# Optimization experiments

Measured on AMD Instinct MI355X. Metric: run time of the kernel, lower is better.

Reference implementation:

```python
import jax, jax.numpy as jnp
import numpy as np

N_NODES = 100000
NFEAT, NHID, NCLASS, HEADS = 256, 16, 40, 8
NEG_SLOPE = 0.2


def gat_conv(x, src, dst, W, att_src, att_dst, bias, n_nodes):
    """PyG-style GATConv (concat heads). x:[N,Fin], src/dst:[E] (self-loops included)."""
    H, C = att_src.shape
    h = (x @ W).reshape(n_nodes, H, C)                      # [N,H,C]
    a_src = jnp.einsum('nhc,hc->nh', h, att_src)            # [N,H]
    a_dst = jnp.einsum('nhc,hc->nh', h, att_dst)            # [N,H]
    e = jax.nn.leaky_relu(a_src[src] + a_dst[dst], NEG_SLOPE)  # [E,H]
    # segment softmax over edges grouped by destination node
    emax = jax.ops.segment_max(e, dst, num_segments=n_nodes)
    emax = jnp.where(jnp.isfinite(emax), emax, 0.0)
    ex = jnp.exp(e - emax[dst])
    denom = jax.ops.segment_sum(ex, dst, num_segments=n_nodes)
    alpha = ex / (denom[dst] + 1e-16)                       # [E,H]
    msg = h[src] * alpha[:, :, None]                        # [E,H,C] gather + weight
    out = jax.ops.segment_sum(msg, dst, num_segments=n_nodes)  # [N,H,C]
    return out.reshape(n_nodes, H * C) + bias


def setup_inputs() -> dict:
    key = jax.random.key(0)
    ks = jax.random.split(key, 12)
    E = 1600000
    x = jax.random.normal(ks[0], (N_NODES, NFEAT), dtype=jnp.float32)
    edge_index = jax.random.randint(ks[1], (2, E), 0, N_NODES, dtype=jnp.int64)
    s = 0.05
    W1 = jax.random.normal(ks[2], (NFEAT, HEADS * NHID), dtype=jnp.float32) * s
    att_src1 = jax.random.normal(ks[3], (HEADS, NHID), dtype=jnp.float32) * s
    att_dst1 = jax.random.normal(ks[4], (HEADS, NHID), dtype=jnp.float32) * s
    b1 = jnp.zeros((HEADS * NHID,), dtype=jnp.float32)
    W2 = jax.random.normal(ks[5], (HEADS * NHID, NCLASS), dtype=jnp.float32) * s
    att_src2 = jax.random.normal(ks[6], (1, NCLASS), dtype=jnp.float32) * s
    att_dst2 = jax.random.normal(ks[7], (1, NCLASS), dtype=jnp.float32) * s
    b2 = jnp.zeros((NCLASS,), dtype=jnp.float32)
    return {"x": x, "edge_index": edge_index, "W1": W1, "att_src1": att_src1,
            "att_dst1": att_dst1, "b1": b1, "W2": W2, "att_src2": att_src2,
            "att_dst2": att_dst2, "b2": b2}


def reference(x, edge_index, W1, att_src1, att_dst1, b1, W2, att_src2, att_dst2, b2):
    n = x.shape[0]
    # PyG GATConv adds self-loops by default
    loop = jnp.arange(n, dtype=edge_index.dtype)
    src = jnp.concatenate([edge_index[0], loop])
    dst = jnp.concatenate([edge_index[1], loop])
    h = gat_conv(x, src, dst, W1, att_src1, att_dst1, b1, n)
    h = jax.nn.relu(h)  # activation='relu'; dropout/bn are identity in eval / use_bn=False
    out = gat_conv(h, src, dst, W2, att_src2, att_dst2, b2, n)
    return out
```

## Files before the change

### kernel.cpp

```cpp
#include <hip/hip_runtime.h>
#include <math.h>

#define KF 256
#define F1 128
#define NH 8
#define NC 16
#define NCLS 40
#define NEG 0.2f
#define BM 64

static __device__ __forceinline__ float lrelu(float v) { return fmaxf(v, NEG * v); }

static __device__ __forceinline__ unsigned bf16r(float a) {
    unsigned u = __float_as_uint(a);
    return (u + 0x7fffu + ((u >> 16) & 1u)) >> 16;
}
static __device__ __forceinline__ unsigned bf16pack2(float a, float b) {
    return bf16r(a) | (bf16r(b) << 16);
}
static __device__ __forceinline__ float2 bf2unpack(unsigned v) {
    float2 r;
    r.x = __uint_as_float(v << 16);
    r.y = __uint_as_float(v & 0xffff0000u);
    return r;
}

typedef __attribute__((ext_vector_type(8))) short bf16x8;
typedef __attribute__((ext_vector_type(4))) float f32x4;

__global__ __launch_bounds__(256) void wprep_kernel(const float* __restrict__ W1,
                                                    unsigned short* __restrict__ wfrag)
{
    int gid = blockIdx.x * 256 + threadIdx.x;
    if (gid >= KF * F1) return;
    int k = gid >> 7, nn = gid & 127;
    int kt = k >> 6, ks = (k >> 5) & 1, oct = (k >> 3) & 3, e = k & 7;
    int nt = nn >> 4, ln = (nn & 15) + 16 * oct;
    int idx = (((kt * 8 + nt) * 2 + ks) * 64 + ln) * 8 + e;
    wfrag[idx] = (unsigned short)bf16r(W1[gid]);
}

__global__ __launch_bounds__(256) void gemm1_kernel(const float* __restrict__ x,
        const unsigned short* __restrict__ wfrag,
        const float* __restrict__ att_src, const float* __restrict__ att_dst,
        unsigned short* __restrict__ h1u, float* __restrict__ a_src, float* __restrict__ a_dst, int n)
{
    __shared__ __align__(16) unsigned short Al[4096];
    __shared__ __align__(16) unsigned short Bl[8192];
    const int t = threadIdx.x;
    const int w = t >> 6, lane = t & 63;
    const int row0 = blockIdx.x * BM;

    f32x4 acc[8];
#pragma unroll
    for (int i = 0; i < 8; ++i) acc[i] = (f32x4){0.f, 0.f, 0.f, 0.f};

    for (int kt = 0; kt < 4; ++kt) {
        {
            const int k4 = t & 15;
            const int ks = k4 >> 3;
            const int oct = (k4 >> 1) & 3;
            const int koff = (k4 & 1) * 4;
#pragma unroll
            for (int it = 0; it < 4; ++it) {
                int r = (t >> 4) + it * 16;
                int gr = row0 + r;
                float4 v = make_float4(0.f, 0.f, 0.f, 0.f);
                if (gr < n) v = *(const float4*)&x[(size_t)gr * KF + kt * 64 + k4 * 4];
                int ln = (r & 15) + 16 * oct;
                int rt = r >> 4;
                int idx = ((rt * 2 + ks) * 64 + ln) * 8 + koff;
                uint2 p;
                p.x = bf16pack2(v.x, v.y);
                p.y = bf16pack2(v.z, v.w);
                *(uint2*)&Al[idx] = p;
            }
        }
        {
            const uint4* src = (const uint4*)wfrag + kt * 1024;
            uint4* dstp = (uint4*)Bl;
#pragma unroll
            for (int i = 0; i < 4; ++i) dstp[t + i * 256] = src[t + i * 256];
        }
        __syncthreads();
        bf16x8 a0 = *(const bf16x8*)&Al[(w * 2 + 0) * 512 + lane * 8];
        bf16x8 a1 = *(const bf16x8*)&Al[(w * 2 + 1) * 512 + lane * 8];
#pragma unroll
        for (int nt = 0; nt < 8; ++nt) {
            bf16x8 b0 = *(const bf16x8*)&Bl[(nt * 2 + 0) * 512 + lane * 8];
            bf16x8 b1 = *(const bf16x8*)&Bl[(nt * 2 + 1) * 512 + lane * 8];
            acc[nt] = __builtin_amdgcn_mfma_f32_16x16x32_bf16(a0, b0, acc[nt], 0, 0, 0);
            acc[nt] = __builtin_amdgcn_mfma_f32_16x16x32_bf16(a1, b1, acc[nt], 0, 0, 0);
        }
        __syncthreads();
    }

    const int col = lane & 15, g = lane >> 4;
    const int rbase = row0 + w * 16 + g * 4;
#pragma unroll
    for (int nt = 0; nt < 8; ++nt) {
        float asv = att_src[nt * 16 + col];
        float adv = att_dst[nt * 16 + col];
#pragma unroll
        for (int reg = 0; reg < 4; ++reg) {
            int row = rbase + reg;
            float hv = acc[nt][reg];
            if (row < n) h1u[(size_t)row * F1 + nt * 16 + col] = (unsigned short)bf16r(hv);
            float ps = hv * asv, pd = hv * adv;
            ps += __shfl_xor(ps, 1); ps += __shfl_xor(ps, 2);
            ps += __shfl_xor(ps, 4); ps += __shfl_xor(ps, 8);
            pd += __shfl_xor(pd, 1); pd += __shfl_xor(pd, 2);
            pd += __shfl_xor(pd, 4); pd += __shfl_xor(pd, 8);
            if (col == 0 && row < n) {
                a_src[row * NH + nt] = ps;
                a_dst[row * NH + nt] = pd;
            }
        }
    }
}

__global__ __launch_bounds__(256) void histrank_kernel(const int* __restrict__ ei, int E, int Etot,
                                                       int* __restrict__ counts,
                                                       int* __restrict__ rank)
{
    const int base = blockIdx.x * 2048 + threadIdx.x;
#pragma unroll
    for (int q = 0; q < 8; ++q) {
        int i = base + q * 256;
        if (i < Etot) {
            int dst = (i < E) ? ei[E + i] : (i - E);
            rank[i] = atomicAdd(&counts[dst], 1);
        }
    }
}

__global__ __launch_bounds__(256) void scan1_kernel(const int* __restrict__ counts,
                                                    int* __restrict__ bsum, int n)
{
    __shared__ int lds[256];
    const int t = threadIdx.x;
    const int base = blockIdx.x * 1024 + t * 4;
    int s = 0;
#pragma unroll
    for (int q = 0; q < 4; ++q) { int i = base + q; if (i < n) s += counts[i]; }
    lds[t] = s;
    __syncthreads();
#pragma unroll
    for (int off = 128; off > 0; off >>= 1) {
        if (t < off) lds[t] += lds[t + off];
        __syncthreads();
    }
    if (t == 0) bsum[blockIdx.x] = lds[0];
}

__global__ __launch_bounds__(256) void scan2_kernel(const int* __restrict__ bsum,
                                                    int* __restrict__ boffs, int nb,
                                                    int* __restrict__ indptr, int n, int Etot)
{
    __shared__ int lds[256];
    const int t = threadIdx.x;
    lds[t] = (t < nb) ? bsum[t] : 0;
    __syncthreads();
    for (int off = 1; off < 256; off <<= 1) {
        int v = (t >= off) ? lds[t - off] : 0;
        __syncthreads();
        lds[t] += v;
        __syncthreads();
    }
    if (t < nb) boffs[t] = (t == 0) ? 0 : lds[t - 1];
    if (t == 0) indptr[n] = Etot;
}

__global__ __launch_bounds__(256) void scan3_kernel(const int* __restrict__ counts,
                                                    const int* __restrict__ boffs,
                                                    int* __restrict__ indptr, int n)
{
    __shared__ int lds[256];
    const int t = threadIdx.x;
    const int base = blockIdx.x * 1024 + t * 4;
    int c[4];
    int s = 0;
#pragma unroll
    for (int q = 0; q < 4; ++q) {
        int i = base + q;
        c[q] = (i < n) ? counts[i] : 0;
        s += c[q];
    }
    lds[t] = s;
    __syncthreads();
    for (int off = 1; off < 256; off <<= 1) {
        int v = (t >= off) ? lds[t - off] : 0;
        __syncthreads();
        lds[t] += v;
        __syncthreads();
    }
    int run = boffs[blockIdx.x] + lds[t] - s;
#pragma unroll
    for (int q = 0; q < 4; ++q) {
        int i = base + q;
        if (i < n) indptr[i] = run;
        run += c[q];
    }
}

__global__ __launch_bounds__(256) void fill_kernel(const int* __restrict__ ei, int E, int Etot,
                                                   const int* __restrict__ indptr,
                                                   const int* __restrict__ rank,
                                                   int* __restrict__ sorted_src)
{
    const int base = blockIdx.x * 2048 + threadIdx.x;
#pragma unroll
    for (int q = 0; q < 8; ++q) {
        int i = base + q * 256;
        if (i < Etot) {
            int src, dst;
            if (i < E) { src = ei[i]; dst = ei[E + i]; }
            else       { src = i - E; dst = i - E; }
            sorted_src[indptr[dst] + rank[i]] = src;
        }
    }
}

__global__ __launch_bounds__(256) void agg1_kernel(const unsigned* __restrict__ h1b,
        const float* __restrict__ a_src, const float* __restrict__ a_dst,
        const int* __restrict__ indptr, const int* __restrict__ ssrc,
        const float* __restrict__ b1, unsigned* __restrict__ out1b, int n)
{
    const int wave = threadIdx.x >> 6, lane = threadIdx.x & 63;
    const int dst = blockIdx.x * 4 + wave;
    if (dst >= n) return;
    const int h = lane >> 3;
    const float ad = a_dst[dst * NH + h];
    const int beg = indptr[dst], end = indptr[dst + 1];
    float s0 = 0.f, s1 = 0.f, s2 = 0.f, s3 = 0.f;
    float ax0 = 0.f, ay0 = 0.f, ax1 = 0.f, ay1 = 0.f;
    float ax2 = 0.f, ay2 = 0.f, ax3 = 0.f, ay3 = 0.f;
    int j = beg;
    for (; j + 4 <= end; j += 4) {
        int sc0 = ssrc[j], sc1 = ssrc[j + 1], sc2 = ssrc[j + 2], sc3 = ssrc[j + 3];
        float as0 = a_src[sc0 * NH + h];
        float as1 = a_src[sc1 * NH + h];
        float as2 = a_src[sc2 * NH + h];
        float as3 = a_src[sc3 * NH + h];
        unsigned v0 = h1b[(size_t)sc0 * 64 + lane];
        unsigned v1 = h1b[(size_t)sc1 * 64 + lane];
        unsigned v2 = h1b[(size_t)sc2 * 64 + lane];
        unsigned v3 = h1b[(size_t)sc3 * 64 + lane];
        float p0 = __expf(lrelu(as0 + ad));
        float p1 = __expf(lrelu(as1 + ad));
        float p2 = __expf(lrelu(as2 + ad));
        float p3 = __expf(lrelu(as3 + ad));
        float2 hv0 = bf2unpack(v0), hv1 = bf2unpack(v1);
        float2 hv2 = bf2unpack(v2), hv3 = bf2unpack(v3);
        s0 += p0; ax0 += p0 * hv0.x; ay0 += p0 * hv0.y;
        s1 += p1; ax1 += p1 * hv1.x; ay1 += p1 * hv1.y;
        s2 += p2; ax2 += p2 * hv2.x; ay2 += p2 * hv2.y;
        s3 += p3; ax3 += p3 * hv3.x; ay3 += p3 * hv3.y;
    }
    for (; j < end; ++j) {
        int sc = ssrc[j];
        float as = a_src[sc * NH + h];
        float2 hv = bf2unpack(h1b[(size_t)sc * 64 + lane]);
        float p = __expf(lrelu(as + ad));
        s0 += p; ax0 += p * hv.x; ay0 += p * hv.y;
    }
    float s = (s0 + s1) + (s2 + s3);
    float accx = (ax0 + ax1) + (ax2 + ax3);
    float accy = (ay0 + ay1) + (ay2 + ay3);
    float inv = 1.f / (s + 1e-16f);
    float2 bb = *(const float2*)&b1[lane * 2];
    float ox = fmaxf(accx * inv + bb.x, 0.f);
    float oy = fmaxf(accy * inv + bb.y, 0.f);
    out1b[(size_t)dst * 64 + lane] = bf16pack2(ox, oy);
}

__global__ __launch_bounds__(256) void gemm2_kernel(const unsigned* __restrict__ out1b,
        const float* __restrict__ W2, const float* __restrict__ atts2,
        const float* __restrict__ attd2,
        unsigned short* __restrict__ h2us, float* __restrict__ a_src, float* __restrict__ a_dst, int n)
{
    __shared__ float wl[128][NCLS];
    __shared__ float xs[64][68];
    const int t = threadIdx.x;
    const int row0 = blockIdx.x * 64;
    const int rg = t >> 3;
    const int cg = t & 7;
    const int r0 = rg * 2;

#pragma unroll
    for (int i = t; i < 1280; i += 256)
        *(float4*)&wl[0][0 + i * 4] = *(const float4*)&W2[i * 4];

    float acc[2][5];
#pragma unroll
    for (int i = 0; i < 2; ++i)
#pragma unroll
        for (int j = 0; j < 5; ++j) acc[i][j] = 0.f;

    for (int kh = 0; kh < 2; ++kh) {
#pragma unroll
        for (int i = t; i < 1024; i += 256) {
            int r = i >> 4, u2 = i & 15;
            int gr = row0 + r;
            float4 v = make_float4(0.f, 0.f, 0.f, 0.f);
            if (gr < n) {
                uint2 pk = *(const uint2*)&out1b[(size_t)gr * 64 + kh * 32 + u2 * 2];
                float2 ab = bf2unpack(pk.x);
                float2 cd = bf2unpack(pk.y);
                v = make_float4(ab.x, ab.y, cd.x, cd.y);
            }
            *(float4*)&xs[r][u2 * 4] = v;
        }
        __syncthreads();
#pragma unroll 4
        for (int k = 0; k < 64; ++k) {
            float xa = xs[r0][k];
            float xb = xs[r0 + 1][k];
            const float* wr = &wl[kh * 64 + k][cg * 5];
#pragma unroll
            for (int j = 0; j < 5; ++j) {
                float w = wr[j];
                acc[0][j] += xa * w;
                acc[1][j] += xb * w;
            }
        }
        __syncthreads();
    }

    float as5[5], ad5[5];
#pragma unroll
    for (int j = 0; j < 5; ++j) {
        as5[j] = atts2[cg * 5 + j];
        ad5[j] = attd2[cg * 5 + j];
    }
#pragma unroll
    for (int i = 0; i < 2; ++i) {
        int row = row0 + r0 + i;
        if (row >= n) break;
#pragma unroll
        for (int j = 0; j < 5; ++j)
            h2us[(size_t)row * NCLS + cg * 5 + j] = (unsigned short)bf16r(acc[i][j]);
        float ps = acc[i][0] * as5[0] + acc[i][1] * as5[1] + acc[i][2] * as5[2]
                 + acc[i][3] * as5[3] + acc[i][4] * as5[4];
        float pd = acc[i][0] * ad5[0] + acc[i][1] * ad5[1] + acc[i][2] * ad5[2]
                 + acc[i][3] * ad5[3] + acc[i][4] * ad5[4];
        ps += __shfl_xor(ps, 1); ps += __shfl_xor(ps, 2); ps += __shfl_xor(ps, 4);
        pd += __shfl_xor(pd, 1); pd += __shfl_xor(pd, 2); pd += __shfl_xor(pd, 4);
        if (cg == 0) { a_src[row] = ps; a_dst[row] = pd; }
    }
}

__global__ __launch_bounds__(256) void agg2_kernel(const unsigned* __restrict__ h2b,
        const float* __restrict__ a_src, const float* __restrict__ a_dst,
        const int* __restrict__ indptr, const int* __restrict__ ssrc,
        const float* __restrict__ b2, float* __restrict__ out, int n)
{
    const int wave = threadIdx.x >> 6, lane = threadIdx.x & 63;
    const int grp = lane / 20;
    const int sub = lane - grp * 20;
    const int dst = blockIdx.x * 12 + wave * 3 + grp;
    const bool valid = (grp < 3) && (dst < n);
    const float ad = valid ? a_dst[dst] : 0.f;
    int beg = 0, end = 0;
    if (valid) { beg = indptr[dst]; end = indptr[dst + 1]; }
    float s0 = 0.f, s1 = 0.f, s2 = 0.f, s3 = 0.f;
    float ax0 = 0.f, ay0 = 0.f, ax1 = 0.f, ay1 = 0.f;
    float ax2 = 0.f, ay2 = 0.f, ax3 = 0.f, ay3 = 0.f;
    int j = beg;
    for (; j + 4 <= end; j += 4) {
        int sc0 = ssrc[j], sc1 = ssrc[j + 1], sc2 = ssrc[j + 2], sc3 = ssrc[j + 3];
        float p0 = __expf(lrelu(a_src[sc0] + ad));
        float p1 = __expf(lrelu(a_src[sc1] + ad));
        float p2 = __expf(lrelu(a_src[sc2] + ad));
        float p3 = __expf(lrelu(a_src[sc3] + ad));
        float2 h0 = bf2unpack(h2b[(size_t)sc0 * 20 + sub]);
        float2 h1v = bf2unpack(h2b[(size_t)sc1 * 20 + sub]);
        float2 h2v = bf2unpack(h2b[(size_t)sc2 * 20 + sub]);
        float2 h3v = bf2unpack(h2b[(size_t)sc3 * 20 + sub]);
        s0 += p0; ax0 += p0 * h0.x;  ay0 += p0 * h0.y;
        s1 += p1; ax1 += p1 * h1v.x; ay1 += p1 * h1v.y;
        s2 += p2; ax2 += p2 * h2v.x; ay2 += p2 * h2v.y;
        s3 += p3; ax3 += p3 * h3v.x; ay3 += p3 * h3v.y;
    }
    for (; j < end; ++j) {
        int sc = ssrc[j];
        float p = __expf(lrelu(a_src[sc] + ad));
        float2 hv = bf2unpack(h2b[(size_t)sc * 20 + sub]);
        s0 += p; ax0 += p * hv.x; ay0 += p * hv.y;
    }
    if (valid) {
        float s = (s0 + s1) + (s2 + s3);
        float accx = (ax0 + ax1) + (ax2 + ax3);
        float accy = (ay0 + ay1) + (ay2 + ay3);
        float inv = 1.f / (s + 1e-16f);
        float2 o;
        o.x = accx * inv + b2[sub * 2];
        o.y = accy * inv + b2[sub * 2 + 1];
        *(float2*)&out[(size_t)dst * NCLS + sub * 2] = o;
    }
}

extern "C" void kernel_launch(void* const* d_in, const int* in_sizes, int n_in,
                              void* d_out, int out_size, void* d_ws, size_t ws_size,
                              hipStream_t stream)
{
    const float* x   = (const float*)d_in[0];
    const int*   ei  = (const int*)d_in[1];
    const float* W1  = (const float*)d_in[2];
    const float* as1 = (const float*)d_in[3];
    const float* ad1 = (const float*)d_in[4];
    const float* b1  = (const float*)d_in[5];
    const float* W2  = (const float*)d_in[6];
    const float* as2 = (const float*)d_in[7];
    const float* ad2 = (const float*)d_in[8];
    const float* b2  = (const float*)d_in[9];
    float* out = (float*)d_out;

    const int n    = in_sizes[0] / KF;
    const int E    = in_sizes[1] / 2;
    const int Etot = E + n;

    char* ws = (char*)d_ws;
    unsigned* h1b   = (unsigned*)ws;
    unsigned* out1b = (unsigned*)(ws + 25600000);
    float* a_s1     = (float*)(ws + 51200000);
    float* a_d1     = (float*)(ws + 54400000);
    int*   indptr   = (int*)  (ws + 57600000);
    int*   counts   = (int*)  (ws + 58000016);
    int*   ssrc     = (int*)  (ws + 58400016);
    unsigned short* wfrag = (unsigned short*)(ws + 65200016);
    int*   rank     = (int*)  (ws + 65270016);
    int*   bsum     = (int*)  (ws + 72070016);
    int*   boffs    = (int*)  (ws + 72074112);
    unsigned* h2b   = (unsigned*)ws;
    float* a_s2     = (float*)(ws + 8000000);
    float* a_d2     = (float*)(ws + 8400000);

    const int nb = (n + 1023) / 1024;
    dim3 b256(256);

    hipMemsetAsync(counts, 0, n * sizeof(int), stream);
    wprep_kernel<<<dim3((KF * F1 + 255) / 256), b256, 0, stream>>>(W1, wfrag);
    gemm1_kernel<<<dim3((n + BM - 1) / BM), b256, 0, stream>>>(x, wfrag, as1, ad1,
                                                               (unsigned short*)h1b, a_s1, a_d1, n);
    histrank_kernel<<<dim3((Etot + 2047) / 2048), b256, 0, stream>>>(ei, E, Etot, counts, rank);
    scan1_kernel<<<dim3(nb), b256, 0, stream>>>(counts, bsum, n);
    scan2_kernel<<<dim3(1), b256, 0, stream>>>(bsum, boffs, nb, indptr, n, Etot);
    scan3_kernel<<<dim3(nb), b256, 0, stream>>>(counts, boffs, indptr, n);
    fill_kernel<<<dim3((Etot + 2047) / 2048), b256, 0, stream>>>(ei, E, Etot, indptr, rank, ssrc);
    agg1_kernel<<<dim3((n + 3) / 4), b256, 0, stream>>>(h1b, a_s1, a_d1, indptr, ssrc, b1, out1b, n);
    gemm2_kernel<<<dim3((n + 63) / 64), b256, 0, stream>>>(out1b, W2, as2, ad2,
                                                           (unsigned short*)h2b, a_s2, a_d2, n);
    agg2_kernel<<<dim3((n + 11) / 12), b256, 0, stream>>>(h2b, a_s2, a_d2, indptr, ssrc, b2, out, n);
}
```

Baseline: 318.1 us.

## Keep W1 fragments in registers and double-buffer x tiles in gemm1

Each wave now loads its two column tiles of W1 once into registers for all K steps, which removes the per-iteration shared-memory staging of B. The x tile is double-buffered in LDS, and the global loads for the next K slice are issued before the MFMAs on the current one, so only one barrier is needed per step. The per-wave split changes from rows to column tiles. This adds register pressure (Breg plus a 4x2 accumulator array), which could lower occupancy.

```diff
diff --git a/kernel.cpp b/kernel.cpp
--- a/kernel.cpp
+++ b/kernel.cpp
@@ -7,7 +7,6 @@
 #define NC 16
 #define NCLS 40
 #define NEG 0.2f
-#define BM 64
 
 static __device__ __forceinline__ float lrelu(float v) { return fmaxf(v, NEG * v); }
 
@@ -45,75 +44,109 @@
         const float* __restrict__ att_src, const float* __restrict__ att_dst,
         unsigned short* __restrict__ h1u, float* __restrict__ a_src, float* __restrict__ a_dst, int n)
 {
-    __shared__ __align__(16) unsigned short Al[4096];
-    __shared__ __align__(16) unsigned short Bl[8192];
+    __shared__ __align__(16) unsigned short Al[2][4096];
     const int t = threadIdx.x;
     const int w = t >> 6, lane = t & 63;
-    const int row0 = blockIdx.x * BM;
-
-    f32x4 acc[8];
-#pragma unroll
-    for (int i = 0; i < 8; ++i) acc[i] = (f32x4){0.f, 0.f, 0.f, 0.f};
-
+    const int row0 = blockIdx.x * 64;
+    const int nt0 = w * 2;
+
+    bf16x8 Breg[4][2][2];
+#pragma unroll
+    for (int kt = 0; kt < 4; ++kt)
+#pragma unroll
+        for (int ntl = 0; ntl < 2; ++ntl)
+#pragma unroll
+            for (int ks = 0; ks < 2; ++ks)
+                Breg[kt][ntl][ks] =
+                    *(const bf16x8*)&wfrag[(((kt * 8 + nt0 + ntl) * 2 + ks) * 64 + lane) * 8];
+
+    const int k4 = t & 15, ks0 = k4 >> 3, oct = (k4 >> 1) & 3, koff = (k4 & 1) * 4;
+    const int rloc = t >> 4;
+    const float4 z4 = make_float4(0.f, 0.f, 0.f, 0.f);
+
+    float4 buf[4];
+#pragma unroll
+    for (int it = 0; it < 4; ++it) {
+        int gr = row0 + rloc + it * 16;
+        buf[it] = (gr < n) ? *(const float4*)&x[(size_t)gr * KF + k4 * 4] : z4;
+    }
+#pragma unroll
+    for (int it = 0; it < 4; ++it) {
+        int r = rloc + it * 16;
+        int ln = (r & 15) + 16 * oct, rt = r >> 4;
+        int idx = ((rt * 2 + ks0) * 64 + ln) * 8 + koff;
+        *(uint2*)&Al[0][idx] = make_uint2(bf16pack2(buf[it].x, buf[it].y),
+                                          bf16pack2(buf[it].z, buf[it].w));
+    }
+    __syncthreads();
+
+    f32x4 acc[4][2];
+#pragma unroll
+    for (int i = 0; i < 4; ++i)
+#pragma unroll
+        for (int j = 0; j < 2; ++j) acc[i][j] = (f32x4){0.f, 0.f, 0.f, 0.f};
+
+#pragma unroll
     for (int kt = 0; kt < 4; ++kt) {
-        {
-            const int k4 = t & 15;
-            const int ks = k4 >> 3;
-            const int oct = (k4 >> 1) & 3;
-            const int koff = (k4 & 1) * 4;
+        const int b = kt & 1;
+        if (kt < 3) {
 #pragma unroll
             for (int it = 0; it < 4; ++it) {
-                int r = (t >> 4) + it * 16;
-                int gr = row0 + r;
-                float4 v = make_float4(0.f, 0.f, 0.f, 0.f);
-                if (gr < n) v = *(const float4*)&x[(size_t)gr * KF + kt * 64 + k4 * 4];
-                int ln = (r & 15) + 16 * oct;
-                int rt = r >> 4;
-                int idx = ((rt * 2 + ks) * 64 + ln) * 8 + koff;
-                uint2 p;
-                p.x = bf16pack2(v.x, v.y);
-                p.y = bf16pack2(v.z, v.w);
-                *(uint2*)&Al[idx] = p;
-            }
-        }
-        {
-            const uint4* src = (const uint4*)wfrag + kt * 1024;
-            uint4* dstp = (uint4*)Bl;
-#pragma unroll
-            for (int i = 0; i < 4; ++i) dstp[t + i * 256] = src[t + i * 256];
-        }
-        __syncthreads();
-        bf16x8 a0 = *(const bf16x8*)&Al[(w * 2 + 0) * 512 + lane * 8];
-        bf16x8 a1 = *(const bf16x8*)&Al[(w * 2 + 1) * 512 + lane * 8];
-#pragma unroll
-        for (int nt = 0; nt < 8; ++nt) {
-            bf16x8 b0 = *(const bf16x8*)&Bl[(nt * 2 + 0) * 512 + lane * 8];
-            bf16x8 b1 = *(const bf16x8*)&Bl[(nt * 2 + 1) * 512 + lane * 8];
-            acc[nt] = __builtin_amdgcn_mfma_f32_16x16x32_bf16(a0, b0, acc[nt], 0, 0, 0);
-            acc[nt] = __builtin_amdgcn_mfma_f32_16x16x32_bf16(a1, b1, acc[nt], 0, 0, 0);
-        }
-        __syncthreads();
+                int gr = row0 + rloc + it * 16;
+                buf[it] = (gr < n) ? *(const float4*)&x[(size_t)gr * KF + (kt + 1) * 64 + k4 * 4] : z4;
+            }
+        }
+        bf16x8 areg[4][2];
+#pragma unroll
+        for (int rg = 0; rg < 4; ++rg)
+#pragma unroll
+            for (int ks = 0; ks < 2; ++ks)
+                areg[rg][ks] = *(const bf16x8*)&Al[b][((rg * 2 + ks) * 64 + lane) * 8];
+#pragma unroll
+        for (int rg = 0; rg < 4; ++rg)
+#pragma unroll
+            for (int ntl = 0; ntl < 2; ++ntl) {
+                acc[rg][ntl] = __builtin_amdgcn_mfma_f32_16x16x32_bf16(
+                    areg[rg][0], Breg[kt][ntl][0], acc[rg][ntl], 0, 0, 0);
+                acc[rg][ntl] = __builtin_amdgcn_mfma_f32_16x16x32_bf16(
+                    areg[rg][1], Breg[kt][ntl][1], acc[rg][ntl], 0, 0, 0);
+            }
+        if (kt < 3) {
+#pragma unroll
+            for (int it = 0; it < 4; ++it) {
+                int r = rloc + it * 16;
+                int ln = (r & 15) + 16 * oct, rt = r >> 4;
+                int idx = ((rt * 2 + ks0) * 64 + ln) * 8 + koff;
+                *(uint2*)&Al[b ^ 1][idx] = make_uint2(bf16pack2(buf[it].x, buf[it].y),
+                                                      bf16pack2(buf[it].z, buf[it].w));
+            }
+            __syncthreads();
+        }
     }
 
     const int col = lane & 15, g = lane >> 4;
-    const int rbase = row0 + w * 16 + g * 4;
-#pragma unroll
-    for (int nt = 0; nt < 8; ++nt) {
-        float asv = att_src[nt * 16 + col];
-        float adv = att_dst[nt * 16 + col];
-#pragma unroll
-        for (int reg = 0; reg < 4; ++reg) {
-            int row = rbase + reg;
-            float hv = acc[nt][reg];
-            if (row < n) h1u[(size_t)row * F1 + nt * 16 + col] = (unsigned short)bf16r(hv);
-            float ps = hv * asv, pd = hv * adv;
-            ps += __shfl_xor(ps, 1); ps += __shfl_xor(ps, 2);
-            ps += __shfl_xor(ps, 4); ps += __shfl_xor(ps, 8);
-            pd += __shfl_xor(pd, 1); pd += __shfl_xor(pd, 2);
-            pd += __shfl_xor(pd, 4); pd += __shfl_xor(pd, 8);
-            if (col == 0 && row < n) {
-                a_src[row * NH + nt] = ps;
-                a_dst[row * NH + nt] = pd;
+#pragma unroll
+    for (int rg = 0; rg < 4; ++rg) {
+        const int rbase = row0 + rg * 16 + g * 4;
+#pragma unroll
+        for (int ntl = 0; ntl < 2; ++ntl) {
+            const int nt = nt0 + ntl;
+            float asv = att_src[nt * 16 + col];
+            float adv = att_dst[nt * 16 + col];
+#pragma unroll
+            for (int reg = 0; reg < 4; ++reg) {
+                int row = rbase + reg;
+                float hv = acc[rg][ntl][reg];
+                if (row < n) h1u[(size_t)row * F1 + nt * 16 + col] = (unsigned short)bf16r(hv);
+                float ps = hv * asv, pd = hv * adv;
+                ps += __shfl_xor(ps, 1); ps += __shfl_xor(ps, 2);
+                ps += __shfl_xor(ps, 4); ps += __shfl_xor(ps, 8);
+                pd += __shfl_xor(pd, 1); pd += __shfl_xor(pd, 2);
+                pd += __shfl_xor(pd, 4); pd += __shfl_xor(pd, 8);
+                if (col == 0 && row < n) {
+                    a_src[row * NH + nt] = ps;
+                    a_dst[row * NH + nt] = pd;
+                }
             }
         }
     }
@@ -441,8 +474,8 @@
 
     hipMemsetAsync(counts, 0, n * sizeof(int), stream);
     wprep_kernel<<<dim3((KF * F1 + 255) / 256), b256, 0, stream>>>(W1, wfrag);
-    gemm1_kernel<<<dim3((n + BM - 1) / BM), b256, 0, stream>>>(x, wfrag, as1, ad1,
-                                                               (unsigned short*)h1b, a_s1, a_d1, n);
+    gemm1_kernel<<<dim3((n + 63) / 64), b256, 0, stream>>>(x, wfrag, as1, ad1,
+                                                           (unsigned short*)h1b, a_s1, a_d1, n);
     histrank_kernel<<<dim3((Etot + 2047) / 2048), b256, 0, stream>>>(ei, E, Etot, counts, rank);
     scan1_kernel<<<dim3(nb), b256, 0, stream>>>(counts, bsum, n);
     scan2_kernel<<<dim3(1), b256, 0, stream>>>(bsum, boffs, nb, indptr, n, Etot);
```

Measured after the change: 334.8 us. 1.05x slower.

## Store layer-1 features head-major and aggregate one head per block

Applied to the files above, without the earlier changes.

The layer-1 features and attention scalars are rewritten head-major ([head][node][16]) so that agg1 can run blocks that each handle one head for 32 destination nodes, with 8 lanes per node. Each head's feature slab (about 3.2 MB) is more likely to stay in cache during the random gathers, and a_src reads become contiguous per head. The cost is that divergent degrees within a wave now force lockstep iteration to the longest neighbour list, and ssrc is re-read once per head. gemm2 is adjusted to read the new layout.

```diff
diff --git a/kernel.cpp b/kernel.cpp
--- a/kernel.cpp
+++ b/kernel.cpp
@@ -43,7 +43,8 @@
 __global__ __launch_bounds__(256) void gemm1_kernel(const float* __restrict__ x,
         const unsigned short* __restrict__ wfrag,
         const float* __restrict__ att_src, const float* __restrict__ att_dst,
-        unsigned short* __restrict__ h1u, float* __restrict__ a_src, float* __restrict__ a_dst, int n)
+        unsigned short* __restrict__ h1h, float* __restrict__ a_srcH, float* __restrict__ a_dstH,
+        int n)
 {
     __shared__ __align__(16) unsigned short Al[4096];
     __shared__ __align__(16) unsigned short Bl[8192];
@@ -101,19 +102,20 @@
     for (int nt = 0; nt < 8; ++nt) {
         float asv = att_src[nt * 16 + col];
         float adv = att_dst[nt * 16 + col];
+        const size_t hb = (size_t)nt * n;
 #pragma unroll
         for (int reg = 0; reg < 4; ++reg) {
             int row = rbase + reg;
             float hv = acc[nt][reg];
-            if (row < n) h1u[(size_t)row * F1 + nt * 16 + col] = (unsigned short)bf16r(hv);
+            if (row < n) h1h[(hb + row) * 16 + col] = (unsigned short)bf16r(hv);
             float ps = hv * asv, pd = hv * adv;
             ps += __shfl_xor(ps, 1); ps += __shfl_xor(ps, 2);
             ps += __shfl_xor(ps, 4); ps += __shfl_xor(ps, 8);
             pd += __shfl_xor(pd, 1); pd += __shfl_xor(pd, 2);
             pd += __shfl_xor(pd, 4); pd += __shfl_xor(pd, 8);
             if (col == 0 && row < n) {
-                a_src[row * NH + nt] = ps;
-                a_dst[row * NH + nt] = pd;
+                a_srcH[hb + row] = ps;
+                a_dstH[hb + row] = pd;
             }
         }
     }
@@ -221,60 +223,67 @@
     }
 }
 
-__global__ __launch_bounds__(256) void agg1_kernel(const unsigned* __restrict__ h1b,
-        const float* __restrict__ a_src, const float* __restrict__ a_dst,
+__global__ __launch_bounds__(256) void agg1_kernel(const unsigned* __restrict__ h1hu,
+        const float* __restrict__ a_srcH, const float* __restrict__ a_dstH,
         const int* __restrict__ indptr, const int* __restrict__ ssrc,
-        const float* __restrict__ b1, unsigned* __restrict__ out1b, int n)
-{
+        const float* __restrict__ b1, unsigned* __restrict__ out1h, int n)
+{
+    const int head = blockIdx.x & 7;
+    const int chunk = blockIdx.x >> 3;
     const int wave = threadIdx.x >> 6, lane = threadIdx.x & 63;
-    const int dst = blockIdx.x * 4 + wave;
-    if (dst >= n) return;
-    const int h = lane >> 3;
-    const float ad = a_dst[dst * NH + h];
-    const int beg = indptr[dst], end = indptr[dst + 1];
+    const int grp = lane >> 3, cl = lane & 7;
+    const int dst = chunk * 32 + wave * 8 + grp;
+    const bool valid = dst < n;
+    const size_t hb = (size_t)head * n;
+    float ad = 0.f;
+    int j = 0, end = 0;
+    if (valid) {
+        ad = a_dstH[hb + dst];
+        j = indptr[dst];
+        end = indptr[dst + 1];
+    }
     float s0 = 0.f, s1 = 0.f, s2 = 0.f, s3 = 0.f;
     float ax0 = 0.f, ay0 = 0.f, ax1 = 0.f, ay1 = 0.f;
     float ax2 = 0.f, ay2 = 0.f, ax3 = 0.f, ay3 = 0.f;
-    int j = beg;
-    for (; j + 4 <= end; j += 4) {
-        int sc0 = ssrc[j], sc1 = ssrc[j + 1], sc2 = ssrc[j + 2], sc3 = ssrc[j + 3];
-        float as0 = a_src[sc0 * NH + h];
-        float as1 = a_src[sc1 * NH + h];
-        float as2 = a_src[sc2 * NH + h];
-        float as3 = a_src[sc3 * NH + h];
-        unsigned v0 = h1b[(size_t)sc0 * 64 + lane];
-        unsigned v1 = h1b[(size_t)sc1 * 64 + lane];
-        unsigned v2 = h1b[(size_t)sc2 * 64 + lane];
-        unsigned v3 = h1b[(size_t)sc3 * 64 + lane];
-        float p0 = __expf(lrelu(as0 + ad));
-        float p1 = __expf(lrelu(as1 + ad));
-        float p2 = __expf(lrelu(as2 + ad));
-        float p3 = __expf(lrelu(as3 + ad));
-        float2 hv0 = bf2unpack(v0), hv1 = bf2unpack(v1);
-        float2 hv2 = bf2unpack(v2), hv3 = bf2unpack(v3);
-        s0 += p0; ax0 += p0 * hv0.x; ay0 += p0 * hv0.y;
-        s1 += p1; ax1 += p1 * hv1.x; ay1 += p1 * hv1.y;
-        s2 += p2; ax2 += p2 * hv2.x; ay2 += p2 * hv2.y;
-        s3 += p3; ax3 += p3 * hv3.x; ay3 += p3 * hv3.y;
-    }
-    for (; j < end; ++j) {
-        int sc = ssrc[j];
-        float as = a_src[sc * NH + h];
-        float2 hv = bf2unpack(h1b[(size_t)sc * 64 + lane]);
-        float p = __expf(lrelu(as + ad));
-        s0 += p; ax0 += p * hv.x; ay0 += p * hv.y;
-    }
-    float s = (s0 + s1) + (s2 + s3);
-    float accx = (ax0 + ax1) + (ax2 + ax3);
-    float accy = (ay0 + ay1) + (ay2 + ay3);
-    float inv = 1.f / (s + 1e-16f);
-    float2 bb = *(const float2*)&b1[lane * 2];
-    float ox = fmaxf(accx * inv + bb.x, 0.f);
-    float oy = fmaxf(accy * inv + bb.y, 0.f);
-    out1b[(size_t)dst * 64 + lane] = bf16pack2(ox, oy);
-}
-
-__global__ __launch_bounds__(256) void gemm2_kernel(const unsigned* __restrict__ out1b,
+    while (__any(j < end)) {
+        bool a0 = j < end, a1 = j + 1 < end, a2 = j + 2 < end, a3 = j + 3 < end;
+        int sc0 = a0 ? ssrc[j]     : 0;
+        int sc1 = a1 ? ssrc[j + 1] : 0;
+        int sc2 = a2 ? ssrc[j + 2] : 0;
+        int sc3 = a3 ? ssrc[j + 3] : 0;
+        float as0 = a_srcH[hb + sc0];
+        float as1 = a_srcH[hb + sc1];
+        float as2 = a_srcH[hb + sc2];
+        float as3 = a_srcH[hb + sc3];
+        unsigned v0 = h1hu[(hb + sc0) * 8 + cl];
+        unsigned v1 = h1hu[(hb + sc1) * 8 + cl];
+        unsigned v2 = h1hu[(hb + sc2) * 8 + cl];
+        unsigned v3 = h1hu[(hb + sc3) * 8 + cl];
+        float p0 = a0 ? __expf(lrelu(as0 + ad)) : 0.f;
+        float p1 = a1 ? __expf(lrelu(as1 + ad)) : 0.f;
+        float p2 = a2 ? __expf(lrelu(as2 + ad)) : 0.f;
+        float p3 = a3 ? __expf(lrelu(as3 + ad)) : 0.f;
+        float2 h0 = bf2unpack(v0), h1v = bf2unpack(v1);
+        float2 h2v = bf2unpack(v2), h3v = bf2unpack(v3);
+        s0 += p0; ax0 += p0 * h0.x;  ay0 += p0 * h0.y;
+        s1 += p1; ax1 += p1 * h1v.x; ay1 += p1 * h1v.y;
+        s2 += p2; ax2 += p2 * h2v.x; ay2 += p2 * h2v.y;
+        s3 += p3; ax3 += p3 * h3v.x; ay3 += p3 * h3v.y;
+        j += 4;
+    }
+    if (valid) {
+        float s = (s0 + s1) + (s2 + s3);
+        float ax = (ax0 + ax1) + (ax2 + ax3);
+        float ay = (ay0 + ay1) + (ay2 + ay3);
+        float inv = 1.f / (s + 1e-16f);
+        float2 bb = *(const float2*)&b1[head * 16 + cl * 2];
+        float ox = fmaxf(ax * inv + bb.x, 0.f);
+        float oy = fmaxf(ay * inv + bb.y, 0.f);
+        out1h[(hb + dst) * 8 + cl] = bf16pack2(ox, oy);
+    }
+}
+
+__global__ __launch_bounds__(256) void gemm2_kernel(const unsigned* __restrict__ out1h,
         const float* __restrict__ W2, const float* __restrict__ atts2,
         const float* __restrict__ attd2,
         unsigned short* __restrict__ h2us, float* __restrict__ a_src, float* __restrict__ a_dst, int n)
@@ -304,7 +313,9 @@
             int gr = row0 + r;
             float4 v = make_float4(0.f, 0.f, 0.f, 0.f);
             if (gr < n) {
-                uint2 pk = *(const uint2*)&out1b[(size_t)gr * 64 + kh * 32 + u2 * 2];
+                int u = kh * 32 + u2 * 2;
+                int hh = u >> 3, cc = u & 7;
+                uint2 pk = *(const uint2*)&out1h[((size_t)hh * n + gr) * 8 + cc];
                 float2 ab = bf2unpack(pk.x);
                 float2 cd = bf2unpack(pk.y);
                 v = make_float4(ab.x, ab.y, cd.x, cd.y);
@@ -448,7 +459,8 @@
     scan2_kernel<<<dim3(1), b256, 0, stream>>>(bsum, boffs, nb, indptr, n, Etot);
     scan3_kernel<<<dim3(nb), b256, 0, stream>>>(counts, boffs, indptr, n);
     fill_kernel<<<dim3((Etot + 2047) / 2048), b256, 0, stream>>>(ei, E, Etot, indptr, rank, ssrc);
-    agg1_kernel<<<dim3((n + 3) / 4), b256, 0, stream>>>(h1b, a_s1, a_d1, indptr, ssrc, b1, out1b, n);
+    agg1_kernel<<<dim3(((n + 31) / 32) * 8), b256, 0, stream>>>(h1b, a_s1, a_d1, indptr, ssrc,
+                                                                b1, out1b, n);
     gemm2_kernel<<<dim3((n + 63) / 64), b256, 0, stream>>>(out1b, W2, as2, ad2,
                                                            (unsigned short*)h2b, a_s2, a_d2, n);
     agg2_kernel<<<dim3((n + 11) / 12), b256, 0, stream>>>(h2b, a_s2, a_d2, indptr, ssrc, b2, out, n);
```

After: 399.9 us. 25.7% more time.
